# Performance work log

Hardware: AMD Instinct MI355X
Metric: run time of the kernel (lower is better)

The kernel has to match this reference:

```python
import jax, jax.numpy as jnp
import numpy as np

EPS = 1e-08


def setup_inputs() -> dict:
    key = jax.random.key(0)
    k1, k2, k3 = jax.random.split(key, 3)
    N, IN_DIM, OUT_DIM = 8192, 512, 512
    h = jax.random.normal(k1, (N, IN_DIM), dtype=jnp.float32)
    adj = jax.random.randint(k2, (N, N), 0, 2, dtype=jnp.int32)
    # nn.Linear(in_dim, out_dim, bias=False) weight: [out_dim, in_dim]
    W = jax.random.normal(k3, (OUT_DIM, IN_DIM), dtype=jnp.float32) * (1.0 / np.sqrt(IN_DIM))
    return {"h": h, "adj": adj, "W": W}


def reference(h, adj, W):
    # Wh = h @ W^T  -> [N, out_dim]
    Wh = h @ W.T
    N = Wh.shape[0]
    norms = jnp.linalg.norm(Wh, axis=1, keepdims=True)  # [N, 1]
    # cosine similarity [N, N]
    sim = (Wh @ Wh.T) / (norms * norms.T + EPS)
    mask = (adj > 0) | jnp.eye(N, dtype=bool)
    sim_masked = jnp.where(mask, sim, -jnp.inf)
    alpha = jax.nn.softmax(sim_masked, axis=1)
    return alpha @ Wh
```

## Files before the change

### kernel.cpp

```cpp
#include <hip/hip_runtime.h>
#include <hip/hip_bf16.h>
#include <stdint.h>

#define NN 8192
#define DD 512

typedef unsigned short u16;
typedef unsigned long long u64;
typedef __attribute__((ext_vector_type(8))) short short8;
typedef __attribute__((ext_vector_type(4))) float f32x4;

__device__ __forceinline__ void gld_lds16(const void* g, void* l) {
  __builtin_amdgcn_global_load_lds(
      (const __attribute__((address_space(1))) uint32_t*)(uintptr_t)g,
      (__attribute__((address_space(3))) uint32_t*)(uintptr_t)l,
      16, 0, 0);
}

__device__ __forceinline__ u16 f2bf(float f) {
  __hip_bfloat16 b = __float2bfloat16(f);
  return __builtin_bit_cast(u16, b);
}

__global__ void fill_kernel(float* __restrict__ p, int n, float v) {
  int i = blockIdx.x * 256 + threadIdx.x;
  int stride = gridDim.x * 256;
  for (; i < n; i += stride) p[i] = v;
}

__global__ void cvt4_kernel(const float4* __restrict__ src, ushort4* __restrict__ dst, int n4) {
  int i = blockIdx.x * 256 + threadIdx.x;
  int stride = gridDim.x * 256;
  for (; i < n4; i += stride) {
    float4 v = src[i];
    ushort4 o;
    o.x = f2bf(v.x); o.y = f2bf(v.y); o.z = f2bf(v.z); o.w = f2bf(v.w);
    dst[i] = o;
  }
}

__global__ void rownorm_kernel(const float* __restrict__ Wh, float* __restrict__ invn,
                               float* __restrict__ den) {
  int row = blockIdx.x;
  int l = threadIdx.x;
  const float4* p = (const float4*)(Wh + (size_t)row * DD);
  float4 a = p[l], b = p[l + 64];
  float s = a.x*a.x + a.y*a.y + a.z*a.z + a.w*a.w
          + b.x*b.x + b.y*b.y + b.z*b.z + b.w*b.w;
  #pragma unroll
  for (int off = 32; off; off >>= 1) s += __shfl_down(s, off);
  if (l == 0) {
    invn[row] = 1.0f / sqrtf(s);
    den[row] = 0.0f;
  }
}

__global__ void u_wht_kernel(const float* __restrict__ Wh, const float* __restrict__ invn,
                             u16* __restrict__ U, u16* __restrict__ WhT) {
  __shared__ float tile[64][65];
  int i0 = blockIdx.x * 64, d0 = blockIdx.y * 64;
  int c = threadIdx.x & 63, rb = threadIdx.x >> 6;
  #pragma unroll
  for (int r = rb; r < 64; r += 4) {
    float v = Wh[(size_t)(i0 + r) * DD + d0 + c];
    tile[r][c] = v;
    U[(size_t)(i0 + r) * DD + d0 + c] = f2bf(v * invn[i0 + r]);
  }
  __syncthreads();
  #pragma unroll
  for (int r = rb; r < 64; r += 4) {
    WhT[(size_t)(d0 + r) * NN + i0 + c] = f2bf(tile[c][r]);
  }
}

__global__ void __launch_bounds__(256) gemm_wh(
    const u16* __restrict__ A, const u16* __restrict__ B,
    int Nn, int K, float* __restrict__ Cf)
{
  __shared__ __align__(16) u16 As[128 * 32];
  __shared__ __align__(16) u16 Bs[128 * 32];

  const int tid = threadIdx.x;
  const int w = tid >> 6;
  const int lane = tid & 63;
  const int lm = lane & 15;
  const int q = lane >> 4;
  const int row0 = blockIdx.y * 128;
  const int col0 = blockIdx.x * 128;
  const int RM = (w >> 1) * 64;
  const int RN = (w & 1) * 64;
  const int sr = tid >> 2;
  const int sk = (tid & 3) * 8;

  f32x4 acc[4][4];
  #pragma unroll
  for (int a_ = 0; a_ < 4; a_++)
    #pragma unroll
    for (int b_ = 0; b_ < 4; b_++)
      acc[a_][b_] = (f32x4){0.f, 0.f, 0.f, 0.f};

  const size_t Abase = (size_t)row0 * K;
  const size_t Bbase = (size_t)col0 * K;

  for (int k0 = 0; k0 < K; k0 += 32) {
    __syncthreads();
    gld_lds16(A + Abase + (size_t)sr * K + k0 + sk,        (char*)As + w * 1024);
    gld_lds16(A + Abase + (size_t)(sr + 64) * K + k0 + sk, (char*)As + 4096 + w * 1024);
    gld_lds16(B + Bbase + (size_t)sr * K + k0 + sk,        (char*)Bs + w * 1024);
    gld_lds16(B + Bbase + (size_t)(sr + 64) * K + k0 + sk, (char*)Bs + 4096 + w * 1024);
    __syncthreads();

    short8 af[4], bfr[4];
    #pragma unroll
    for (int mt = 0; mt < 4; mt++)
      af[mt] = *(const short8*)&As[(RM + mt * 16 + lm) * 32 + q * 8];
    #pragma unroll
    for (int nt = 0; nt < 4; nt++)
      bfr[nt] = *(const short8*)&Bs[(RN + nt * 16 + lm) * 32 + q * 8];

    #pragma unroll
    for (int mt = 0; mt < 4; mt++)
      #pragma unroll
      for (int nt = 0; nt < 4; nt++)
        acc[mt][nt] = __builtin_amdgcn_mfma_f32_16x16x32_bf16(af[mt], bfr[nt], acc[mt][nt], 0, 0, 0);
  }

  #pragma unroll
  for (int mt = 0; mt < 4; mt++) {
    const int ib = row0 + RM + mt * 16 + q * 4;
    #pragma unroll
    for (int rr = 0; rr < 4; rr++) {
      const int i = ib + rr;
      #pragma unroll
      for (int nt = 0; nt < 4; nt++) {
        const int jc = col0 + RN + nt * 16 + lm;
        Cf[(size_t)i * Nn + jc] = acc[mt][nt][rr];
      }
    }
  }
}

__global__ void __launch_bounds__(256) gemm_sim(
    const u16* __restrict__ U, const int* __restrict__ adj,
    u16* __restrict__ Pb, float* __restrict__ den)
{
  __shared__ __align__(16) char lds[32768];

  const int b = blockIdx.x;
  int bi = (int)((sqrtf(8.0f * (float)b + 1.0f) - 1.0f) * 0.5f);
  while ((bi + 1) * (bi + 2) / 2 <= b) bi++;
  while (bi * (bi + 1) / 2 > b) bi--;
  const int bj = b - bi * (bi + 1) / 2;

  const int tid = threadIdx.x;
  const int w = tid >> 6;
  const int lane = tid & 63;
  const int lm = lane & 15;
  const int q = lane >> 4;
  const int row0 = bi * 128;
  const int col0 = bj * 128;
  const int RM = (w >> 1) * 64;
  const int RN = (w & 1) * 64;
  const bool diag = (bi == bj);

  const u16* Ab = U + (size_t)row0 * DD;
  const u16* Bb = U + (size_t)col0 * DD;

  const int srow = tid >> 2;
  const int sch8 = (((tid & 3) ^ ((tid >> 3) & 3)) << 3);
  const int wofs = w << 10;

  const int rA = RM + lm;
  const int rB = RN + lm;
  const int aoff = rA * 64 + ((q ^ ((rA >> 1) & 3)) << 4);
  const int boff = 8192 + rB * 64 + ((q ^ ((rB >> 1) & 3)) << 4);

  f32x4 acc[4][4];
  #pragma unroll
  for (int a_ = 0; a_ < 4; a_++)
    #pragma unroll
    for (int b_ = 0; b_ < 4; b_++)
      acc[a_][b_] = (f32x4){0.f, 0.f, 0.f, 0.f};

#define SSTAGE(koff, dstoff)                                                      \
  do {                                                                            \
    char* d_ = lds + (dstoff);                                                    \
    gld_lds16(Ab + (size_t)srow * DD + (koff) + sch8,        d_ + wofs);          \
    gld_lds16(Ab + (size_t)(srow + 64) * DD + (koff) + sch8, d_ + 4096 + wofs);   \
    gld_lds16(Bb + (size_t)srow * DD + (koff) + sch8,        d_ + 8192 + wofs);   \
    gld_lds16(Bb + (size_t)(srow + 64) * DD + (koff) + sch8, d_ + 12288 + wofs);  \
  } while (0)

  SSTAGE(0, 0);
  SSTAGE(32, 16384);
  asm volatile("s_waitcnt vmcnt(4)" ::: "memory");
  asm volatile("s_barrier" ::: "memory");

#define STILE(T, CBOFF)                                                           \
  do {                                                                            \
    const char* cb = lds + (CBOFF);                                               \
    short8 af[4], bfr[4];                                                         \
    _Pragma("unroll")                                                             \
    for (int m = 0; m < 4; m++)                                                   \
      af[m] = *(const short8*)(cb + aoff + m * 1024);                             \
    _Pragma("unroll")                                                             \
    for (int n = 0; n < 4; n++)                                                   \
      bfr[n] = *(const short8*)(cb + boff + n * 1024);                            \
    asm volatile("s_barrier" ::: "memory");                                       \
    asm volatile("s_waitcnt lgkmcnt(0)" ::: "memory");                            \
    __builtin_amdgcn_s_setprio(1);                                                \
    _Pragma("unroll")                                                             \
    for (int m = 0; m < 2; m++)                                                   \
      _Pragma("unroll")                                                           \
      for (int n = 0; n < 4; n++)                                                 \
        acc[m][n] = __builtin_amdgcn_mfma_f32_16x16x32_bf16(af[m], bfr[n], acc[m][n], 0, 0, 0); \
    __builtin_amdgcn_s_setprio(0);                                                \
    asm volatile("s_barrier" ::: "memory");                                       \
    if ((T) + 2 < 16) SSTAGE(((T) + 2) * 32, CBOFF);                              \
    asm volatile("s_barrier" ::: "memory");                                       \
    __builtin_amdgcn_s_setprio(1);                                                \
    _Pragma("unroll")                                                             \
    for (int m = 2; m < 4; m++)                                                   \
      _Pragma("unroll")                                                           \
      for (int n = 0; n < 4; n++)                                                 \
        acc[m][n] = __builtin_amdgcn_mfma_f32_16x16x32_bf16(af[m], bfr[n], acc[m][n], 0, 0, 0); \
    __builtin_amdgcn_s_setprio(0);                                                \
    if ((T) + 2 < 16) { asm volatile("s_waitcnt vmcnt(4)" ::: "memory"); }        \
    else              { asm volatile("s_waitcnt vmcnt(0)" ::: "memory"); }        \
    asm volatile("s_barrier" ::: "memory");                                       \
  } while (0)

  #pragma unroll 1
  for (int t = 0; t < 16; t += 2) {
    STILE(t, 0);
    STILE(t + 1, 16384);
  }
#undef STILE
#undef SSTAGE

  float msum[4] = {0.f, 0.f, 0.f, 0.f};

  #pragma unroll
  for (int mt = 0; mt < 4; mt++) {
    const int ibase = row0 + RM + mt * 16 + q * 4;

    int na[4][4];
    #pragma unroll
    for (int rr = 0; rr < 4; rr++)
      #pragma unroll
      for (int nt = 0; nt < 4; nt++)
        na[rr][nt] = adj[(size_t)(ibase + rr) * NN + col0 + RN + nt * 16 + lm];
    uint4 ma[4];
    if (!diag) {
      #pragma unroll
      for (int nt = 0; nt < 4; nt++)
        ma[nt] = *(const uint4*)&adj[(size_t)(col0 + RN + nt * 16 + lm) * NN + ibase];
    }

    float pm[4][4];
    #pragma unroll
    for (int rr = 0; rr < 4; rr++) {
      const int i = ibase + rr;
      float psum = 0.f;
      #pragma unroll
      for (int nt = 0; nt < 4; nt++) {
        const int jc = col0 + RN + nt * 16 + lm;
        const float ev = __expf(acc[mt][nt][rr]);
        const bool on = (na[rr][nt] != 0) || (diag && i == jc);
        const float p = on ? ev : 0.0f;
        psum += p;
        Pb[(size_t)i * NN + jc] = f2bf(p);
        if (!diag) {
          const unsigned mv = (rr == 0) ? ma[nt].x : (rr == 1) ? ma[nt].y
                            : (rr == 2) ? ma[nt].z : ma[nt].w;
          const float pmv = (mv != 0u) ? ev : 0.0f;
          pm[nt][rr] = pmv;
          msum[nt] += pmv;
        }
      }
      #pragma unroll
      for (int off = 8; off; off >>= 1) psum += __shfl_down(psum, off, 16);
      if (lm == 0) atomicAdd(&den[i], psum);
    }
    if (!diag) {
      #pragma unroll
      for (int nt = 0; nt < 4; nt++) {
        const int jc = col0 + RN + nt * 16 + lm;
        ushort4 m4;
        m4.x = f2bf(pm[nt][0]); m4.y = f2bf(pm[nt][1]);
        m4.z = f2bf(pm[nt][2]); m4.w = f2bf(pm[nt][3]);
        *(ushort4*)&Pb[(size_t)jc * NN + ibase] = m4;
      }
    }
  }

  if (!diag) {
    #pragma unroll
    for (int nt = 0; nt < 4; nt++) {
      float s = msum[nt];
      s += __shfl_xor(s, 16);
      s += __shfl_xor(s, 32);
      if (q == 0) atomicAdd(&den[col0 + RN + nt * 16 + lm], s);
    }
  }
}

__global__ void __launch_bounds__(512, 2) gemm_out2(
    const u16* __restrict__ P_,
    const u16* __restrict__ Wt,
    u16* __restrict__ p0, u16* __restrict__ p1,
    u16* __restrict__ p2, u16* __restrict__ p3)
{
  __shared__ __align__(16) char lds[65536];

  const int tid = threadIdx.x;
  const int lane = tid & 63;
  const int lm = lane & 15;
  const int q = lane >> 4;
  const int w = tid >> 6;
  const int wm = w >> 2;
  const int wn = w & 3;
  const int row0 = blockIdx.x * 256;
  const int col0 = blockIdx.y * 256;
  const int z = blockIdx.z;
  const int kBegin = z * (NN / 4);
  const int NT = (NN / 4) / 32;

  const u16* Ab = P_ + (size_t)row0 * NN;
  const u16* Bb = Wt + (size_t)col0 * NN;

  const int srow = tid >> 2;
  const int sch8 = (((tid & 3) ^ ((tid >> 3) & 3)) << 3);
  const int wofs = (tid >> 6) << 10;

  const int rA = wm * 128 + lm;
  const int rB = wn * 64 + lm;
  const int aoff = rA * 64 + ((q ^ ((rA >> 1) & 3)) << 4);
  const int boff = 16384 + rB * 64 + ((q ^ ((rB >> 1) & 3)) << 4);

  f32x4 acc[8][4];
  #pragma unroll
  for (int m = 0; m < 8; m++)
    #pragma unroll
    for (int n = 0; n < 4; n++)
      acc[m][n] = (f32x4){0.f, 0.f, 0.f, 0.f};

#define STAGE4(koff, dstoff)                                                      \
  do {                                                                            \
    char* d_ = lds + (dstoff);                                                    \
    gld_lds16(Ab + (size_t)srow * NN + (koff) + sch8,         d_ + wofs);         \
    gld_lds16(Ab + (size_t)(srow + 128) * NN + (koff) + sch8, d_ + 8192 + wofs);  \
    gld_lds16(Bb + (size_t)srow * NN + (koff) + sch8,         d_ + 16384 + wofs); \
    gld_lds16(Bb + (size_t)(srow + 128) * NN + (koff) + sch8, d_ + 24576 + wofs); \
  } while (0)

  STAGE4(kBegin, 0);
  STAGE4(kBegin + 32, 32768);
  asm volatile("s_waitcnt vmcnt(4)" ::: "memory");
  asm volatile("s_barrier" ::: "memory");

#define TILE(T, CBOFF)                                                            \
  do {                                                                            \
    const char* cb = lds + (CBOFF);                                               \
    short8 af[8], bf_[4];                                                         \
    _Pragma("unroll")                                                             \
    for (int m = 0; m < 8; m++)                                                   \
      af[m] = *(const short8*)(cb + aoff + m * 1024);                             \
    _Pragma("unroll")                                                             \
    for (int n = 0; n < 4; n++)                                                   \
      bf_[n] = *(const short8*)(cb + boff + n * 1024);                            \
    asm volatile("s_barrier" ::: "memory");                                       \
    asm volatile("s_waitcnt lgkmcnt(0)" ::: "memory");                            \
    __builtin_amdgcn_s_setprio(1);                                                \
    _Pragma("unroll")                                                             \
    for (int m = 0; m < 4; m++)                                                   \
      _Pragma("unroll")                                                           \
      for (int n = 0; n < 4; n++)                                                 \
        acc[m][n] = __builtin_amdgcn_mfma_f32_16x16x32_bf16(af[m], bf_[n], acc[m][n], 0, 0, 0); \
    __builtin_amdgcn_s_setprio(0);                                                \
    asm volatile("s_barrier" ::: "memory");                                       \
    if ((T) + 2 < NT) STAGE4(kBegin + ((T) + 2) * 32, CBOFF);                     \
    asm volatile("s_barrier" ::: "memory");                                       \
    __builtin_amdgcn_s_setprio(1);                                                \
    _Pragma("unroll")                                                             \
    for (int m = 4; m < 8; m++)                                                   \
      _Pragma("unroll")                                                           \
      for (int n = 0; n < 4; n++)                                                 \
        acc[m][n] = __builtin_amdgcn_mfma_f32_16x16x32_bf16(af[m], bf_[n], acc[m][n], 0, 0, 0); \
    __builtin_amdgcn_s_setprio(0);                                                \
    if ((T) + 2 < NT) { asm volatile("s_waitcnt vmcnt(4)" ::: "memory"); }        \
    else              { asm volatile("s_waitcnt vmcnt(0)" ::: "memory"); }        \
    asm volatile("s_barrier" ::: "memory");                                       \
  } while (0)

  #pragma unroll 1
  for (int t = 0; t < NT; t += 2) {
    TILE(t, 0);
    TILE(t + 1, 32768);
  }
#undef TILE
#undef STAGE4

  u16* const part = (z == 0) ? p0 : (z == 1) ? p1 : (z == 2) ? p2 : p3;
  #pragma unroll
  for (int m = 0; m < 8; m++) {
    const int ib = row0 + wm * 128 + m * 16 + q * 4;
    #pragma unroll
    for (int rr = 0; rr < 4; rr++) {
      const int i = ib + rr;
      #pragma unroll
      for (int n = 0; n < 4; n++) {
        const int dc = col0 + wn * 64 + n * 16 + lm;
        part[(size_t)i * DD + dc] = f2bf(acc[m][n][rr]);
      }
    }
  }
}

__global__ void reduce4_kernel(const uint4* __restrict__ p0, const uint4* __restrict__ p1,
                               const uint4* __restrict__ p2, const uint4* __restrict__ p3,
                               const float* __restrict__ den, float4* __restrict__ out) {
  const int idx = blockIdx.x * 256 + threadIdx.x;
  const int row = idx >> 6;
  const float dinv = 1.0f / den[row];
  float s[8] = {0, 0, 0, 0, 0, 0, 0, 0};
  #pragma unroll
  for (int zp = 0; zp < 4; zp++) {
    const uint4 u = (zp == 0 ? p0 : zp == 1 ? p1 : zp == 2 ? p2 : p3)[idx];
    s[0] += __uint_as_float(u.x << 16); s[1] += __uint_as_float(u.x & 0xffff0000u);
    s[2] += __uint_as_float(u.y << 16); s[3] += __uint_as_float(u.y & 0xffff0000u);
    s[4] += __uint_as_float(u.z << 16); s[5] += __uint_as_float(u.z & 0xffff0000u);
    s[6] += __uint_as_float(u.w << 16); s[7] += __uint_as_float(u.w & 0xffff0000u);
  }
  float4 o0 = {s[0] * dinv, s[1] * dinv, s[2] * dinv, s[3] * dinv};
  float4 o1 = {s[4] * dinv, s[5] * dinv, s[6] * dinv, s[7] * dinv};
  out[idx * 2] = o0;
  out[idx * 2 + 1] = o1;
}

extern "C" void kernel_launch(void* const* d_in, const int* in_sizes, int n_in,
                              void* d_out, int out_size, void* d_ws, size_t ws_size,
                              hipStream_t stream) {
  const float* h = (const float*)d_in[0];
  const int* adj = (const int*)d_in[1];
  const float* W = (const float*)d_in[2];
  float* out = (float*)d_out;

  const size_t SZ_P    = (size_t)NN * NN * 2;
  const size_t SZ_MASK = (size_t)NN * NN / 8;
  const size_t SZ_WHT  = (size_t)DD * NN * 2;
  const size_t SZ_HB   = (size_t)NN * DD * 2;
  const size_t SZ_WB   = (size_t)DD * DD * 2;
  const size_t SZ_U    = (size_t)NN * DD * 2;
  const size_t SZ_P3   = (size_t)NN * DD * 2;
  const size_t NEEDED  = SZ_P + SZ_MASK + SZ_WHT + SZ_HB + SZ_WB + SZ_U + SZ_P3 + 2 * (size_t)NN * 4;

  if (ws_size < NEEDED) {
    fill_kernel<<<256, 256, 0, stream>>>(out, out_size, 12345.0f);
    return;
  }

  char* ws = (char*)d_ws;
  size_t off = 0;
  u16*   P    = (u16*)(ws + off); off += SZ_P;
  u16*   mask = (u16*)(ws + off); off += SZ_MASK;
  u16*   WhT  = (u16*)(ws + off); off += SZ_WHT;
  u16*   hb   = (u16*)(ws + off); off += SZ_HB;
  u16*   Wb   = (u16*)(ws + off); off += SZ_WB;
  u16*   U    = (u16*)(ws + off); off += SZ_U;
  u16*   p3   = (u16*)(ws + off); off += SZ_P3;
  float* invn = (float*)(ws + off);
  float* den  = invn + NN;

  float* Wh = (float*)P;
  u16* part0 = mask;
  u16* part1 = U;
  u16* part2 = hb;
  u16* part3 = p3;

  cvt4_kernel<<<1024, 256, 0, stream>>>((const float4*)h, (ushort4*)hb, NN * DD / 4);
  cvt4_kernel<<<256, 256, 0, stream>>>((const float4*)W, (ushort4*)Wb, DD * DD / 4);
  gemm_wh<<<dim3(DD / 128, NN / 128), 256, 0, stream>>>(hb, Wb, DD, DD, Wh);
  rownorm_kernel<<<NN, 64, 0, stream>>>(Wh, invn, den);
  u_wht_kernel<<<dim3(NN / 64, DD / 64), 256, 0, stream>>>(Wh, invn, U, WhT);
  gemm_sim<<<64 * 65 / 2, 256, 0, stream>>>(U, adj, P, den);
  gemm_out2<<<dim3(NN / 256, DD / 256, 4), 512, 0, stream>>>(P, WhT, part0, part1, part2, part3);
  reduce4_kernel<<<NN * DD / 8 / 256, 256, 0, stream>>>(
      (const uint4*)part0, (const uint4*)part1, (const uint4*)part2, (const uint4*)part3,
      den, (float4*)out);
}
```

Measured before the change: 579.8 us.

## Compute full similarity grid instead of triangle and prefetch adjacency in epilogue

```diff
diff --git a/kernel.cpp b/kernel.cpp
--- a/kernel.cpp
+++ b/kernel.cpp
@@ -6,7 +6,6 @@
 #define DD 512
 
 typedef unsigned short u16;
-typedef unsigned long long u64;
 typedef __attribute__((ext_vector_type(8))) short short8;
 typedef __attribute__((ext_vector_type(4))) float f32x4;
 
@@ -146,11 +145,8 @@
 {
   __shared__ __align__(16) char lds[32768];
 
-  const int b = blockIdx.x;
-  int bi = (int)((sqrtf(8.0f * (float)b + 1.0f) - 1.0f) * 0.5f);
-  while ((bi + 1) * (bi + 2) / 2 <= b) bi++;
-  while (bi * (bi + 1) / 2 > b) bi--;
-  const int bj = b - bi * (bi + 1) / 2;
+  const int bj = blockIdx.x;
+  const int bi = blockIdx.y;
 
   const int tid = threadIdx.x;
   const int w = tid >> 6;
@@ -182,6 +178,17 @@
     for (int b_ = 0; b_ < 4; b_++)
       acc[a_][b_] = (f32x4){0.f, 0.f, 0.f, 0.f};
 
+  int na0[4][4], na1[4][4];
+  {
+    const int ib0 = row0 + RM + q * 4;
+    #pragma unroll
+    for (int rr = 0; rr < 4; rr++)
+      #pragma unroll
+      for (int nt = 0; nt < 4; nt++)
+        na0[rr][nt] = adj[(size_t)(ib0 + rr) * NN + col0 + RN + nt * 16 + lm];
+  }
+  asm volatile("" ::: "memory");
+
 #define SSTAGE(koff, dstoff)                                                      \
   do {                                                                            \
     char* d_ = lds + (dstoff);                                                    \
@@ -238,71 +245,41 @@
 #undef STILE
 #undef SSTAGE
 
-  float msum[4] = {0.f, 0.f, 0.f, 0.f};
-
-  #pragma unroll
-  for (int mt = 0; mt < 4; mt++) {
-    const int ibase = row0 + RM + mt * 16 + q * 4;
-
-    int na[4][4];
-    #pragma unroll
-    for (int rr = 0; rr < 4; rr++)
-      #pragma unroll
-      for (int nt = 0; nt < 4; nt++)
-        na[rr][nt] = adj[(size_t)(ibase + rr) * NN + col0 + RN + nt * 16 + lm];
-    uint4 ma[4];
-    if (!diag) {
-      #pragma unroll
-      for (int nt = 0; nt < 4; nt++)
-        ma[nt] = *(const uint4*)&adj[(size_t)(col0 + RN + nt * 16 + lm) * NN + ibase];
-    }
-
-    float pm[4][4];
-    #pragma unroll
-    for (int rr = 0; rr < 4; rr++) {
-      const int i = ibase + rr;
-      float psum = 0.f;
-      #pragma unroll
-      for (int nt = 0; nt < 4; nt++) {
-        const int jc = col0 + RN + nt * 16 + lm;
-        const float ev = __expf(acc[mt][nt][rr]);
-        const bool on = (na[rr][nt] != 0) || (diag && i == jc);
-        const float p = on ? ev : 0.0f;
-        psum += p;
-        Pb[(size_t)i * NN + jc] = f2bf(p);
-        if (!diag) {
-          const unsigned mv = (rr == 0) ? ma[nt].x : (rr == 1) ? ma[nt].y
-                            : (rr == 2) ? ma[nt].z : ma[nt].w;
-          const float pmv = (mv != 0u) ? ev : 0.0f;
-          pm[nt][rr] = pmv;
-          msum[nt] += pmv;
-        }
-      }
-      #pragma unroll
-      for (int off = 8; off; off >>= 1) psum += __shfl_down(psum, off, 16);
-      if (lm == 0) atomicAdd(&den[i], psum);
-    }
-    if (!diag) {
-      #pragma unroll
-      for (int nt = 0; nt < 4; nt++) {
-        const int jc = col0 + RN + nt * 16 + lm;
-        ushort4 m4;
-        m4.x = f2bf(pm[nt][0]); m4.y = f2bf(pm[nt][1]);
-        m4.z = f2bf(pm[nt][2]); m4.w = f2bf(pm[nt][3]);
-        *(ushort4*)&Pb[(size_t)jc * NN + ibase] = m4;
-      }
-    }
-  }
-
-  if (!diag) {
-    #pragma unroll
-    for (int nt = 0; nt < 4; nt++) {
-      float s = msum[nt];
-      s += __shfl_xor(s, 16);
-      s += __shfl_xor(s, 32);
-      if (q == 0) atomicAdd(&den[col0 + RN + nt * 16 + lm], s);
-    }
-  }
+#define EPI(MT, NAC, NAN, DOLOAD)                                                 \
+  do {                                                                            \
+    if (DOLOAD) {                                                                 \
+      const int ibn = row0 + RM + ((MT) + 1) * 16 + q * 4;                        \
+      _Pragma("unroll")                                                           \
+      for (int rr = 0; rr < 4; rr++)                                              \
+        _Pragma("unroll")                                                         \
+        for (int nt = 0; nt < 4; nt++)                                            \
+          NAN[rr][nt] = adj[(size_t)(ibn + rr) * NN + col0 + RN + nt * 16 + lm];  \
+    }                                                                             \
+    const int ibc = row0 + RM + (MT) * 16 + q * 4;                                \
+    _Pragma("unroll")                                                             \
+    for (int rr = 0; rr < 4; rr++) {                                              \
+      const int i = ibc + rr;                                                     \
+      float psum = 0.f;                                                           \
+      _Pragma("unroll")                                                           \
+      for (int nt = 0; nt < 4; nt++) {                                            \
+        const int jc = col0 + RN + nt * 16 + lm;                                  \
+        const float ev = __expf(acc[MT][nt][rr]);                                 \
+        const bool on = (NAC[rr][nt] != 0) || (diag && i == jc);                  \
+        const float p = on ? ev : 0.0f;                                           \
+        psum += p;                                                                \
+        Pb[(size_t)i * NN + jc] = f2bf(p);                                        \
+      }                                                                           \
+      _Pragma("unroll")                                                           \
+      for (int off = 8; off; off >>= 1) psum += __shfl_down(psum, off, 16);       \
+      if (lm == 0) atomicAdd(&den[i], psum);                                      \
+    }                                                                             \
+  } while (0)
+
+  EPI(0, na0, na1, 1);
+  EPI(1, na1, na0, 1);
+  EPI(2, na0, na1, 1);
+  EPI(3, na1, na0, 0);
+#undef EPI
 }
 
 __global__ void __launch_bounds__(512, 2) gemm_out2(
@@ -447,13 +424,13 @@
   float* out = (float*)d_out;
 
   const size_t SZ_P    = (size_t)NN * NN * 2;
-  const size_t SZ_MASK = (size_t)NN * NN / 8;
+  const size_t SZ_X0   = (size_t)NN * NN / 8;
   const size_t SZ_WHT  = (size_t)DD * NN * 2;
   const size_t SZ_HB   = (size_t)NN * DD * 2;
   const size_t SZ_WB   = (size_t)DD * DD * 2;
   const size_t SZ_U    = (size_t)NN * DD * 2;
   const size_t SZ_P3   = (size_t)NN * DD * 2;
-  const size_t NEEDED  = SZ_P + SZ_MASK + SZ_WHT + SZ_HB + SZ_WB + SZ_U + SZ_P3 + 2 * (size_t)NN * 4;
+  const size_t NEEDED  = SZ_P + SZ_X0 + SZ_WHT + SZ_HB + SZ_WB + SZ_U + SZ_P3 + 2 * (size_t)NN * 4;
 
   if (ws_size < NEEDED) {
     fill_kernel<<<256, 256, 0, stream>>>(out, out_size, 12345.0f);
@@ -463,7 +440,7 @@
   char* ws = (char*)d_ws;
   size_t off = 0;
   u16*   P    = (u16*)(ws + off); off += SZ_P;
-  u16*   mask = (u16*)(ws + off); off += SZ_MASK;
+  u16*   x0   = (u16*)(ws + off); off += SZ_X0;
   u16*   WhT  = (u16*)(ws + off); off += SZ_WHT;
   u16*   hb   = (u16*)(ws + off); off += SZ_HB;
   u16*   Wb   = (u16*)(ws + off); off += SZ_WB;
@@ -473,7 +450,7 @@
   float* den  = invn + NN;
 
   float* Wh = (float*)P;
-  u16* part0 = mask;
+  u16* part0 = x0;
   u16* part1 = U;
   u16* part2 = hb;
   u16* part3 = p3;
@@ -483,7 +460,7 @@
   gemm_wh<<<dim3(DD / 128, NN / 128), 256, 0, stream>>>(hb, Wb, DD, DD, Wh);
   rownorm_kernel<<<NN, 64, 0, stream>>>(Wh, invn, den);
   u_wht_kernel<<<dim3(NN / 64, DD / 64), 256, 0, stream>>>(Wh, invn, U, WhT);
-  gemm_sim<<<64 * 65 / 2, 256, 0, stream>>>(U, adj, P, den);
+  gemm_sim<<<dim3(NN / 128, NN / 128), 256, 0, stream>>>(U, adj, P, den);
   gemm_out2<<<dim3(NN / 256, DD / 256, 4), 512, 0, stream>>>(P, WhT, part0, part1, part2, part3);
   reduce4_kernel<<<NN * DD / 8 / 256, 256, 0, stream>>>(
       (const uint4*)part0, (const uint4*)part1, (const uint4*)part2, (const uint4*)part3,
```

Result: no change. 569.3 us (-1.8%).
